# Optimization experiments

Hardware: AMD Instinct MI355X
Metric: run time of the kernel (lower is better)

## Reference

```python
import jax, jax.numpy as jnp
import numpy as np

H = 1024        # hidden_size
E = 8           # num_experts
K = 2           # top_k
FF = 4 * H      # expert hidden dim
B, S = 2, 2048


def setup_inputs() -> dict:
    key = jax.random.key(0)
    ks = jax.random.split(key, 7)
    scale = 0.02
    x = jax.random.normal(ks[0], (B, S, H), dtype=jnp.float32)
    Wg = jax.random.normal(ks[1], (H, E), dtype=jnp.float32) * scale
    bg = jnp.zeros((E,), dtype=jnp.float32)
    W1 = jax.random.normal(ks[2], (E, H, FF), dtype=jnp.float32) * scale
    b1 = jnp.zeros((E, FF), dtype=jnp.float32)
    W2 = jax.random.normal(ks[3], (E, FF, H), dtype=jnp.float32) * scale
    b2 = jnp.zeros((E, H), dtype=jnp.float32)
    return {"x": x, "Wg": Wg, "bg": bg, "W1": W1, "b1": b1, "W2": W2, "b2": b2}


def reference(x, Wg, bg, W1, b1, W2, b2):
    b, s, h = x.shape
    xf = x.reshape(-1, h)                                  # [T, H]
    T = xf.shape[0]
    # gating: softmax -> top-k -> renormalize
    probs = jax.nn.softmax(xf @ Wg + bg, axis=-1)          # [T, E]
    vals, idx = jax.lax.top_k(probs, K)                    # [T, K]
    vals = vals / jnp.sum(vals, axis=-1, keepdims=True)
    # dense combine weights: zero for non-selected experts (equivalent math)
    combine = jnp.zeros((T, E), dtype=x.dtype)
    combine = combine.at[jnp.arange(T)[:, None], idx].set(vals)  # [T, E]
    # all-expert FFN (GEMM-dominated), combined with sparse gate weights
    hmid = jax.nn.gelu(jnp.einsum('th,ehf->tef', xf, W1) + b1, approximate=False)  # [T,E,FF]
    y = jnp.einsum('tef,efh->teh', hmid, W2) + b2          # [T, E, H]
    out = jnp.einsum('te,teh->th', combine, y)             # [T, H]
    return out.reshape(b, s, h)
```

## Files before the change

kernel.cpp:

```cpp
#include <hip/hip_runtime.h>
#include <hip/hip_bf16.h>
#include <math.h>

#define T_TOK  4096
#define H_DIM  1024
#define E_NUM  8
#define FF_DIM 4096
#define KSEL   2
#define SLOTS  (T_TOK*KSEL)
#define SLOTS_PAD (SLOTS + 256)
#define BM 128
#define MAXTILES 72

typedef __attribute__((ext_vector_type(8))) short s16x8;
typedef __attribute__((ext_vector_type(8))) unsigned short u16x8;
typedef __attribute__((ext_vector_type(4))) float f32x4;

typedef __attribute__((address_space(1))) const void global_cvoid;
typedef __attribute__((address_space(3))) void lds_void;

__device__ __forceinline__ unsigned short f2bf(float f){
  unsigned int u = __float_as_uint(f);
  u += 0x7fffu + ((u>>16)&1u);
  return (unsigned short)(u>>16);
}
__device__ __forceinline__ float bf2f(unsigned short h){
  return __uint_as_float(((unsigned int)h)<<16);
}

static constexpr size_t OFF_CNT   = 0;
static constexpr size_t OFF_OFFS  = 256;
static constexpr size_t OFF_NT    = 512;
static constexpr size_t OFF_TILES = 768;
static constexpr size_t OFF_IDX   = 1280;
static constexpr size_t OFF_POS   = OFF_IDX  + 32768;
static constexpr size_t OFF_WV    = OFF_POS  + 32768;
static constexpr size_t OFF_SLOT  = OFF_WV   + 32768;
static constexpr size_t OFF_TOK   = OFF_SLOT + 32768;
static constexpr size_t OFF_WOF   = OFF_TOK  + 32768;
static constexpr size_t OFF_XG    = OFF_WOF  + 32768;
static constexpr size_t OFF_W1T   = OFF_XG  + (size_t)SLOTS_PAD*H_DIM*2;
static constexpr size_t OFF_W2T   = OFF_W1T + (size_t)E_NUM*H_DIM*FF_DIM*2;
static constexpr size_t OFF_MID   = OFF_W2T + (size_t)E_NUM*H_DIM*FF_DIM*2;
static constexpr size_t OFF_Y     = OFF_MID + (size_t)SLOTS_PAD*FF_DIM*2;

__global__ __launch_bounds__(64) void gate_kernel(
    const float* __restrict__ x, const float* __restrict__ Wg,
    const float* __restrict__ bg, int* __restrict__ cnt,
    int* __restrict__ idxp, int* __restrict__ posp, float* __restrict__ wvp)
{
  int t = blockIdx.x, lane = threadIdx.x;
  const float* xr = x + (size_t)t*H_DIM;
  float acc[E_NUM];
  #pragma unroll
  for (int e=0;e<E_NUM;e++) acc[e]=0.f;
  for (int i=0;i<H_DIM/64;i++){
    int h = i*64 + lane;
    float xv = xr[h];
    const float* wr_ = Wg + (size_t)h*E_NUM;
    #pragma unroll
    for (int e=0;e<E_NUM;e++) acc[e] += xv*wr_[e];
  }
  #pragma unroll
  for (int e=0;e<E_NUM;e++){
    #pragma unroll
    for (int off=32; off>0; off>>=1) acc[e] += __shfl_xor(acc[e], off);
  }
  if (lane==0){
    float l[E_NUM];
    #pragma unroll
    for (int e=0;e<E_NUM;e++) l[e] = acc[e] + bg[e];
    int i0 = 0;
    #pragma unroll
    for (int e=1;e<E_NUM;e++) if (l[e] > l[i0]) i0 = e;
    int i1 = (i0==0)?1:0;
    #pragma unroll
    for (int e=0;e<E_NUM;e++) if (e!=i0 && l[e] > l[i1]) i1 = e;
    float p1 = expf(l[i1]-l[i0]);
    float s  = 1.f + p1;
    float w0 = 1.f/s, w1 = p1/s;
    int pos0 = atomicAdd(&cnt[i0],1);
    int pos1 = atomicAdd(&cnt[i1],1);
    idxp[t*2]=i0; idxp[t*2+1]=i1;
    posp[t*2]=pos0; posp[t*2+1]=pos1;
    wvp[t*2]=w0; wvp[t*2+1]=w1;
  }
}

__global__ void plan_kernel(const int* __restrict__ cnt, int* __restrict__ offs,
                            int* __restrict__ tiles, int* __restrict__ ntiles)
{
  int o=0, n=0;
  for (int e=0;e<E_NUM;e++){
    offs[e]=o;
    int c=cnt[e];
    int nt=(c+BM-1)/BM;
    for (int m=0;m<nt;m++) tiles[n++] = (e<<16)|m;
    o+=c;
  }
  offs[E_NUM]=o;
  *ntiles=n;
}

__global__ void scatter_kernel(const int* __restrict__ idxp, const int* __restrict__ posp,
                               const float* __restrict__ wvp, const int* __restrict__ offs,
                               int* __restrict__ tok_of, float* __restrict__ w_of,
                               int* __restrict__ slot_of)
{
  int i = blockIdx.x*blockDim.x + threadIdx.x;
  if (i >= SLOTS) return;
  int t = i>>1, k = i&1;
  int e = idxp[t*2+k];
  int slot = offs[e] + posp[t*2+k];
  tok_of[slot] = t;
  w_of[slot]   = wvp[t*2+k];
  slot_of[t*2+k] = slot;
}

__global__ __launch_bounds__(256) void gather_kernel(
    const float* __restrict__ x, const int* __restrict__ tok_of,
    unsigned short* __restrict__ Xg)
{
  int slot = blockIdx.x;
  int t = tok_of[slot];
  const float4* src = (const float4*)(x + (size_t)t*H_DIM);
  float4 v = src[threadIdx.x];
  ushort4 o;
  o.x=f2bf(v.x); o.y=f2bf(v.y); o.z=f2bf(v.z); o.w=f2bf(v.w);
  ((ushort4*)(Xg + (size_t)slot*H_DIM))[threadIdx.x] = o;
}

__global__ __launch_bounds__(256) void transconv_kernel(
    const float* __restrict__ in, unsigned short* __restrict__ out, int R, int C)
{
  __shared__ float tile[64][65];
  int e = blockIdx.z;
  const float* inp = in + (size_t)e*R*C;
  unsigned short* op = out + (size_t)e*R*C;
  int c0 = blockIdx.x*64, r0 = blockIdx.y*64;
  int tx = threadIdx.x & 15, ty = threadIdx.x >> 4;
  #pragma unroll
  for (int i=0;i<4;i++){
    int r = i*16 + ty;
    float4 v = *(const float4*)(inp + (size_t)(r0+r)*C + c0 + tx*4);
    tile[r][tx*4+0]=v.x; tile[r][tx*4+1]=v.y; tile[r][tx*4+2]=v.z; tile[r][tx*4+3]=v.w;
  }
  __syncthreads();
  int wx = threadIdx.x & 7;
  int wcl = threadIdx.x >> 3;
  #pragma unroll
  for (int i=0;i<2;i++){
    int c = i*32 + wcl;
    u16x8 o;
    #pragma unroll
    for (int j=0;j<8;j++) o[j] = f2bf(tile[wx*8+j][c]);
    *(u16x8*)(op + (size_t)(c0+c)*R + r0 + wx*8) = o;
  }
}

#define GLDS(g, l) __builtin_amdgcn_global_load_lds((global_cvoid*)(g), (lds_void*)(l), 16, 0, 0)

template<int MODE>
__global__ __launch_bounds__(256, 4) void gemm128_kernel(
    const unsigned short* __restrict__ A,
    const unsigned short* __restrict__ Bt,
    const float* __restrict__ bias,
    unsigned short* __restrict__ Out,
    const int* __restrict__ tiles, const int* __restrict__ ntiles,
    const int* __restrict__ cnt, const int* __restrict__ offs,
    const float* __restrict__ w_of,
    int N, int K, int cpcs)
{
  int L = blockIdx.x;
  int xcd = L & 7;
  int slot = L >> 3;
  int within = slot & 15;
  int chunk = ((slot >> 4) << 3) + xcd;
  int tb = chunk >> cpcs;
  int cb = chunk & ((1<<cpcs)-1);
  int tile_id = tb*4 + (within & 3);
  if (tile_id >= *ntiles) return;
  int col0 = (cb*4 + (within >> 2)) << 7;

  int packed = tiles[tile_id];
  int e = packed>>16, mt = packed & 0xffff;
  int row0 = offs[e] + mt*BM;
  int nvalid = cnt[e] - mt*BM; if (nvalid > BM) nvalid = BM;
  const unsigned short* Be = Bt + (size_t)e*N*K;

  __shared__ unsigned short As[2][128*32];
  __shared__ unsigned short Bs[2][128*32];
  char* asb = (char*)&As[0][0];
  char* bsb = (char*)&Bs[0][0];

  int t = threadIdx.x;
  int wid = t>>6, lane = t&63;
  int wr = (wid>>1)*64, wc = (wid&1)*64;
  int fr = lane&15, fq = lane>>4;

  int srow = t>>2;
  int sclog = ((t&3) - ((t>>3)&3)) & 3;
  int sdst = wid*1024;

  const unsigned short* gA0 = A  + (size_t)(row0 + srow)*K      + sclog*8;
  const unsigned short* gA1 = A  + (size_t)(row0 + 64 + srow)*K + sclog*8;
  const unsigned short* gB0 = Be + (size_t)(col0 + srow)*K      + sclog*8;
  const unsigned short* gB1 = Be + (size_t)(col0 + 64 + srow)*K + sclog*8;

  auto stage = [&](int buf, int kelem){
    GLDS(gA0 + kelem, asb + buf*8192 + sdst);
    GLDS(gA1 + kelem, asb + buf*8192 + 4096 + sdst);
    GLDS(gB0 + kelem, bsb + buf*8192 + sdst);
    GLDS(gB1 + kelem, bsb + buf*8192 + 4096 + sdst);
  };

  int rd_sw = ((fq + ((fr>>1)&3)) & 3) << 4;

  f32x4 acc[4][4];
  #pragma unroll
  for (int i=0;i<4;i++)
    #pragma unroll
    for (int j=0;j<4;j++) acc[i][j] = (f32x4){0.f,0.f,0.f,0.f};

  int NT = K >> 5;
  stage(0, 0);
  stage(1, 32);
  for (int kt=0; kt<NT; ++kt){
    int cur = kt&1;
    if (kt+1 < NT) asm volatile("s_waitcnt vmcnt(4)" ::: "memory");
    else           asm volatile("s_waitcnt vmcnt(0)" ::: "memory");
    __builtin_amdgcn_s_barrier();
    asm volatile("" ::: "memory");

    s16x8 af[4], bfr[4];
    #pragma unroll
    for (int i=0;i<4;i++){
      af[i]  = *(const s16x8*)(asb + cur*8192 + (wr + i*16 + fr)*64 + rd_sw);
      bfr[i] = *(const s16x8*)(bsb + cur*8192 + (wc + i*16 + fr)*64 + rd_sw);
    }
    #pragma unroll
    for (int i=0;i<4;i++)
      #pragma unroll
      for (int j=0;j<4;j++)
        acc[i][j] = __builtin_amdgcn_mfma_f32_16x16x32_bf16(af[i], bfr[j], acc[i][j], 0,0,0);

    asm volatile("s_waitcnt lgkmcnt(0)" ::: "memory");
    __builtin_amdgcn_s_barrier();
    asm volatile("" ::: "memory");
    if (kt+2 < NT) stage(cur, (kt+2)*32);
  }

  #pragma unroll
  for (int i=0;i<4;i++){
    #pragma unroll
    for (int r=0;r<4;r++){
      int lrow = wr + i*16 + fq*4 + r;
      if (lrow < nvalid){
        int grow = row0 + lrow;
        float scale = (MODE==1) ? w_of[grow] : 0.f;
        #pragma unroll
        for (int j=0;j<4;j++){
          int col = col0 + wc + j*16 + fr;
          float v = acc[i][j][r] + bias[(size_t)e*N + col];
          if (MODE==0) v = 0.5f*v*(1.f + erff(v*0.70710678118654752f));
          else         v *= scale;
          Out[(size_t)grow*N + col] = f2bf(v);
        }
      }
    }
  }
}

__global__ __launch_bounds__(256) void combine_kernel(
    const unsigned short* __restrict__ y, const int* __restrict__ slot_of,
    float* __restrict__ out)
{
  int tok = blockIdx.x;
  int s0 = slot_of[tok*2], s1 = slot_of[tok*2+1];
  const ushort4* y0 = (const ushort4*)(y + (size_t)s0*H_DIM);
  const ushort4* y1 = (const ushort4*)(y + (size_t)s1*H_DIM);
  float4* o = (float4*)(out + (size_t)tok*H_DIM);
  ushort4 a = y0[threadIdx.x], b = y1[threadIdx.x];
  float4 r;
  r.x = bf2f(a.x)+bf2f(b.x);
  r.y = bf2f(a.y)+bf2f(b.y);
  r.z = bf2f(a.z)+bf2f(b.z);
  r.w = bf2f(a.w)+bf2f(b.w);
  o[threadIdx.x] = r;
}

extern "C" void kernel_launch(void* const* d_in, const int* in_sizes, int n_in,
                              void* d_out, int out_size, void* d_ws, size_t ws_size,
                              hipStream_t stream) {
  const float* x  = (const float*)d_in[0];
  const float* Wg = (const float*)d_in[1];
  const float* bg = (const float*)d_in[2];
  const float* W1 = (const float*)d_in[3];
  const float* b1 = (const float*)d_in[4];
  const float* W2 = (const float*)d_in[5];
  const float* b2 = (const float*)d_in[6];
  float* out = (float*)d_out;
  char* ws = (char*)d_ws;

  int*   cnt      = (int*)  (ws + OFF_CNT);
  int*   offs     = (int*)  (ws + OFF_OFFS);
  int*   ntiles   = (int*)  (ws + OFF_NT);
  int*   tiles    = (int*)  (ws + OFF_TILES);
  int*   idxp     = (int*)  (ws + OFF_IDX);
  int*   posp     = (int*)  (ws + OFF_POS);
  float* wvp      = (float*)(ws + OFF_WV);
  int*   slot_of  = (int*)  (ws + OFF_SLOT);
  int*   tok_of   = (int*)  (ws + OFF_TOK);
  float* w_of     = (float*)(ws + OFF_WOF);
  unsigned short* Xg  = (unsigned short*)(ws + OFF_XG);
  unsigned short* W1t = (unsigned short*)(ws + OFF_W1T);
  unsigned short* W2t = (unsigned short*)(ws + OFF_W2T);
  unsigned short* mid = (unsigned short*)(ws + OFF_MID);
  unsigned short* y   = (unsigned short*)(ws + OFF_Y);

  hipMemsetAsync(ws + OFF_CNT, 0, 32, stream);

  gate_kernel<<<T_TOK, 64, 0, stream>>>(x, Wg, bg, cnt, idxp, posp, wvp);
  plan_kernel<<<1, 1, 0, stream>>>(cnt, offs, tiles, ntiles);
  scatter_kernel<<<SLOTS/256, 256, 0, stream>>>(idxp, posp, wvp, offs, tok_of, w_of, slot_of);
  gather_kernel<<<SLOTS, 256, 0, stream>>>(x, tok_of, Xg);

  transconv_kernel<<<dim3(FF_DIM/64, H_DIM/64, E_NUM), 256, 0, stream>>>(W1, W1t, H_DIM, FF_DIM);
  transconv_kernel<<<dim3(H_DIM/64, FF_DIM/64, E_NUM), 256, 0, stream>>>(W2, W2t, FF_DIM, H_DIM);

  gemm128_kernel<0><<<dim3(2304), 256, 0, stream>>>(
      Xg, W1t, b1, mid, tiles, ntiles, cnt, offs, nullptr, FF_DIM, H_DIM, 3);
  gemm128_kernel<1><<<dim3(640), 256, 0, stream>>>(
      mid, W2t, b2, y, tiles, ntiles, cnt, offs, w_of, H_DIM, FF_DIM, 1);

  combine_kernel<<<T_TOK, 256, 0, stream>>>(y, slot_of, out);
}
```

Baseline: 445.5 us.

## Fuse weight transposes, batch gate tokens, tanh-approx GELU, hoist bias loads

Merges the two weight transpose-convert launches into one kernel and has each gate block process four tokens instead of one. In the GEMM it raises the occupancy hint to 5, hoists the bias loads out of the epilogue loop, and swaps exact erf GELU for a tanh-style approximation built from a fast exp. The approximation changes numerics slightly, and the higher occupancy target may force register spills.

New measurement: 766.1 us. 72.0% more time.

```diff
diff --git a/kernel.cpp b/kernel.cpp
--- a/kernel.cpp
+++ b/kernel.cpp
@@ -49,41 +49,44 @@
     const float* __restrict__ bg, int* __restrict__ cnt,
     int* __restrict__ idxp, int* __restrict__ posp, float* __restrict__ wvp)
 {
-  int t = blockIdx.x, lane = threadIdx.x;
-  const float* xr = x + (size_t)t*H_DIM;
-  float acc[E_NUM];
-  #pragma unroll
-  for (int e=0;e<E_NUM;e++) acc[e]=0.f;
-  for (int i=0;i<H_DIM/64;i++){
-    int h = i*64 + lane;
-    float xv = xr[h];
-    const float* wr_ = Wg + (size_t)h*E_NUM;
-    #pragma unroll
-    for (int e=0;e<E_NUM;e++) acc[e] += xv*wr_[e];
-  }
-  #pragma unroll
-  for (int e=0;e<E_NUM;e++){
-    #pragma unroll
-    for (int off=32; off>0; off>>=1) acc[e] += __shfl_xor(acc[e], off);
-  }
-  if (lane==0){
-    float l[E_NUM];
-    #pragma unroll
-    for (int e=0;e<E_NUM;e++) l[e] = acc[e] + bg[e];
-    int i0 = 0;
-    #pragma unroll
-    for (int e=1;e<E_NUM;e++) if (l[e] > l[i0]) i0 = e;
-    int i1 = (i0==0)?1:0;
-    #pragma unroll
-    for (int e=0;e<E_NUM;e++) if (e!=i0 && l[e] > l[i1]) i1 = e;
-    float p1 = expf(l[i1]-l[i0]);
-    float s  = 1.f + p1;
-    float w0 = 1.f/s, w1 = p1/s;
-    int pos0 = atomicAdd(&cnt[i0],1);
-    int pos1 = atomicAdd(&cnt[i1],1);
-    idxp[t*2]=i0; idxp[t*2+1]=i1;
-    posp[t*2]=pos0; posp[t*2+1]=pos1;
-    wvp[t*2]=w0; wvp[t*2+1]=w1;
+  int lane = threadIdx.x;
+  for (int tt=0; tt<4; ++tt){
+    int t = blockIdx.x*4 + tt;
+    const float* xr = x + (size_t)t*H_DIM;
+    float acc[E_NUM];
+    #pragma unroll
+    for (int e=0;e<E_NUM;e++) acc[e]=0.f;
+    for (int i=0;i<H_DIM/64;i++){
+      int h = i*64 + lane;
+      float xv = xr[h];
+      const float* wr_ = Wg + (size_t)h*E_NUM;
+      #pragma unroll
+      for (int e=0;e<E_NUM;e++) acc[e] += xv*wr_[e];
+    }
+    #pragma unroll
+    for (int e=0;e<E_NUM;e++){
+      #pragma unroll
+      for (int off=32; off>0; off>>=1) acc[e] += __shfl_xor(acc[e], off);
+    }
+    if (lane==0){
+      float l[E_NUM];
+      #pragma unroll
+      for (int e=0;e<E_NUM;e++) l[e] = acc[e] + bg[e];
+      int i0 = 0;
+      #pragma unroll
+      for (int e=1;e<E_NUM;e++) if (l[e] > l[i0]) i0 = e;
+      int i1 = (i0==0)?1:0;
+      #pragma unroll
+      for (int e=0;e<E_NUM;e++) if (e!=i0 && l[e] > l[i1]) i1 = e;
+      float p1 = expf(l[i1]-l[i0]);
+      float s  = 1.f + p1;
+      float w0 = 1.f/s, w1 = p1/s;
+      int pos0 = atomicAdd(&cnt[i0],1);
+      int pos1 = atomicAdd(&cnt[i1],1);
+      idxp[t*2]=i0; idxp[t*2+1]=i1;
+      posp[t*2]=pos0; posp[t*2+1]=pos1;
+      wvp[t*2]=w0; wvp[t*2+1]=w1;
+    }
   }
 }
 
@@ -130,14 +133,26 @@
   ((ushort4*)(Xg + (size_t)slot*H_DIM))[threadIdx.x] = o;
 }
 
-__global__ __launch_bounds__(256) void transconv_kernel(
-    const float* __restrict__ in, unsigned short* __restrict__ out, int R, int C)
+__global__ __launch_bounds__(256) void transconv2_kernel(
+    const float* __restrict__ W1, unsigned short* __restrict__ W1t,
+    const float* __restrict__ W2, unsigned short* __restrict__ W2t)
 {
   __shared__ float tile[64][65];
-  int e = blockIdx.z;
+  int id = blockIdx.x;
+  const float* in; unsigned short* out; int R, C, cx, cy, e;
+  if (id < 8192){
+    e = id >> 10; int rem = id & 1023;
+    cx = rem & 63; cy = rem >> 6;
+    R = H_DIM; C = FF_DIM; in = W1; out = W1t;
+  } else {
+    int id2 = id - 8192;
+    e = id2 >> 10; int rem = id2 & 1023;
+    cx = rem & 15; cy = rem >> 4;
+    R = FF_DIM; C = H_DIM; in = W2; out = W2t;
+  }
   const float* inp = in + (size_t)e*R*C;
   unsigned short* op = out + (size_t)e*R*C;
-  int c0 = blockIdx.x*64, r0 = blockIdx.y*64;
+  int c0 = cx*64, r0 = cy*64;
   int tx = threadIdx.x & 15, ty = threadIdx.x >> 4;
   #pragma unroll
   for (int i=0;i<4;i++){
@@ -161,7 +176,7 @@
 #define GLDS(g, l) __builtin_amdgcn_global_load_lds((global_cvoid*)(g), (lds_void*)(l), 16, 0, 0)
 
 template<int MODE>
-__global__ __launch_bounds__(256, 4) void gemm128_kernel(
+__global__ __launch_bounds__(256, 5) void gemm128_kernel(
     const unsigned short* __restrict__ A,
     const unsigned short* __restrict__ Bt,
     const float* __restrict__ bias,
@@ -199,19 +214,19 @@
   int fr = lane&15, fq = lane>>4;
 
   int srow = t>>2;
-  int sclog = ((t&3) - ((t>>3)&3)) & 3;
+  int scl  = ((t&3) - ((t>>3)&3)) & 3;
   int sdst = wid*1024;
 
-  const unsigned short* gA0 = A  + (size_t)(row0 + srow)*K      + sclog*8;
-  const unsigned short* gA1 = A  + (size_t)(row0 + 64 + srow)*K + sclog*8;
-  const unsigned short* gB0 = Be + (size_t)(col0 + srow)*K      + sclog*8;
-  const unsigned short* gB1 = Be + (size_t)(col0 + 64 + srow)*K + sclog*8;
+  const unsigned short* pA0 = A  + (size_t)(row0 + srow)*K      + scl*8;
+  const unsigned short* pA1 = A  + (size_t)(row0 + 64 + srow)*K + scl*8;
+  const unsigned short* pB0 = Be + (size_t)(col0 + srow)*K      + scl*8;
+  const unsigned short* pB1 = Be + (size_t)(col0 + 64 + srow)*K + scl*8;
 
   auto stage = [&](int buf, int kelem){
-    GLDS(gA0 + kelem, asb + buf*8192 + sdst);
-    GLDS(gA1 + kelem, asb + buf*8192 + 4096 + sdst);
-    GLDS(gB0 + kelem, bsb + buf*8192 + sdst);
-    GLDS(gB1 + kelem, bsb + buf*8192 + 4096 + sdst);
+    GLDS(pA0 + kelem, asb + buf*8192 + sdst);
+    GLDS(pA1 + kelem, asb + buf*8192 + 4096 + sdst);
+    GLDS(pB0 + kelem, bsb + buf*8192 + sdst);
+    GLDS(pB1 + kelem, bsb + buf*8192 + 4096 + sdst);
   };
 
   int rd_sw = ((fq + ((fr>>1)&3)) & 3) << 4;
@@ -250,6 +265,9 @@
     if (kt+2 < NT) stage(cur, (kt+2)*32);
   }
 
+  float bias_v[4];
+  #pragma unroll
+  for (int j=0;j<4;j++) bias_v[j] = bias[(size_t)e*N + col0 + wc + j*16 + fr];
   #pragma unroll
   for (int i=0;i<4;i++){
     #pragma unroll
@@ -261,9 +279,14 @@
         #pragma unroll
         for (int j=0;j<4;j++){
           int col = col0 + wc + j*16 + fr;
-          float v = acc[i][j][r] + bias[(size_t)e*N + col];
-          if (MODE==0) v = 0.5f*v*(1.f + erff(v*0.70710678118654752f));
-          else         v *= scale;
+          float v = acc[i][j][r] + bias_v[j];
+          if (MODE==0){
+            float u = v*(0.7978845608f + 0.0356774081f*v*v);
+            float z = __expf(2.f*u);
+            v = v - __fdividef(v, z + 1.f);
+          } else {
+            v *= scale;
+          }
           Out[(size_t)grow*N + col] = f2bf(v);
         }
       }
@@ -320,13 +343,12 @@
 
   hipMemsetAsync(ws + OFF_CNT, 0, 32, stream);
 
-  gate_kernel<<<T_TOK, 64, 0, stream>>>(x, Wg, bg, cnt, idxp, posp, wvp);
+  gate_kernel<<<T_TOK/4, 64, 0, stream>>>(x, Wg, bg, cnt, idxp, posp, wvp);
   plan_kernel<<<1, 1, 0, stream>>>(cnt, offs, tiles, ntiles);
   scatter_kernel<<<SLOTS/256, 256, 0, stream>>>(idxp, posp, wvp, offs, tok_of, w_of, slot_of);
   gather_kernel<<<SLOTS, 256, 0, stream>>>(x, tok_of, Xg);
 
-  transconv_kernel<<<dim3(FF_DIM/64, H_DIM/64, E_NUM), 256, 0, stream>>>(W1, W1t, H_DIM, FF_DIM);
-  transconv_kernel<<<dim3(H_DIM/64, FF_DIM/64, E_NUM), 256, 0, stream>>>(W2, W2t, FF_DIM, H_DIM);
+  transconv2_kernel<<<dim3(16384), 256, 0, stream>>>(W1, W1t, W2, W2t);
 
   gemm128_kernel<0><<<dim3(2304), 256, 0, stream>>>(
       Xg, W1t, b1, mid, tiles, ntiles, cnt, offs, nullptr, FF_DIM, H_DIM, 3);
```
